# Kernel optimization log

Measured on AMD Instinct MI355X. Metric: run time of the kernel, lower is better.

The kernel has to match this reference:

```python
import jax, jax.numpy as jnp
import numpy as np

EMBED_DIM = 1024
NUM_HEADS = 16
HEAD_DIM = EMBED_DIM // NUM_HEADS
N, S = 4, 2048


def setup_inputs() -> dict:
    key = jax.random.key(0)
    ks = jax.random.split(key, 11)
    s = 1.0 / np.sqrt(EMBED_DIM)
    inp = {
        'query': jax.random.normal(ks[0], (N, S, EMBED_DIM), jnp.float32),
        'key': jax.random.normal(ks[1], (N, S, EMBED_DIM), jnp.float32),
        'value': jax.random.normal(ks[2], (N, S, EMBED_DIM), jnp.float32),
        'wq': jax.random.normal(ks[3], (EMBED_DIM, EMBED_DIM), jnp.float32) * s,
        'bq': jnp.zeros((EMBED_DIM,), jnp.float32),
        'wk': jax.random.normal(ks[4], (EMBED_DIM, EMBED_DIM), jnp.float32) * s,
        'bk': jnp.zeros((EMBED_DIM,), jnp.float32),
        'wv': jax.random.normal(ks[5], (EMBED_DIM, EMBED_DIM), jnp.float32) * s,
        'bv': jnp.zeros((EMBED_DIM,), jnp.float32),
        'wo': jax.random.normal(ks[6], (EMBED_DIM, EMBED_DIM), jnp.float32) * s,
        'bo': jnp.zeros((EMBED_DIM,), jnp.float32),
    }
    return inp


def reference(query, key, value, wq, bq, wk, bk, wv, bv, wo, bo):
    n = query.shape[0]
    # projections: y = x @ W^T + b (torch nn.Linear convention)
    Q = query @ wq.T + bq
    K = key @ wk.T + bk
    V = value @ wv.T + bv
    # [n, h, s, d]
    Q = Q.reshape(n, -1, NUM_HEADS, HEAD_DIM).transpose(0, 2, 1, 3)
    K = K.reshape(n, -1, NUM_HEADS, HEAD_DIM).transpose(0, 2, 1, 3)
    V = V.reshape(n, -1, NUM_HEADS, HEAD_DIM).transpose(0, 2, 1, 3)
    energy = jnp.einsum('nhqd,nhkd->nhqk', Q, K)
    attn = jax.nn.softmax(energy / jnp.sqrt(jnp.float32(HEAD_DIM)), axis=-1)
    out = jnp.einsum('nhqk,nhkd->nhqd', attn, V)
    out = out.transpose(0, 2, 1, 3).reshape(n, -1, NUM_HEADS * HEAD_DIM)
    return out @ wo.T + bo
```

## Files before the change

### kernel.cpp

```cpp
#include <hip/hip_runtime.h>
#include <hip/hip_bf16.h>

#define EMBED 1024
#define SEQ   2048
#define NB    4
#define NH    16
#define HD    64
#define MROWS (NB*SEQ)

typedef __attribute__((ext_vector_type(4))) float  f32x4;
typedef __attribute__((ext_vector_type(8))) short  s16x8;

#define MFMA16(a,b,c) __builtin_amdgcn_mfma_f32_16x16x32_bf16((a),(b),(c),0,0,0)

__device__ __forceinline__ unsigned short f2bf(float f) {
    union { float f; unsigned int u; } v; v.f = f;
    unsigned int r = v.u + 0x7fffu + ((v.u >> 16) & 1u);
    return (unsigned short)(r >> 16);
}
__device__ __forceinline__ unsigned int cvtpk(float a, float b) {
    unsigned int r;
    asm("v_cvt_pk_bf16_f32 %0, %1, %2" : "=v"(r) : "v"(a), "v"(b));
    return r;
}
__device__ __forceinline__ float exp2r(float x) {
    float r;
    asm("v_exp_f32 %0, %1" : "=v"(r) : "v"(x));
    return r;
}
__device__ __forceinline__ int swz(int row, int colb) {
    return row*128 + (colb ^ ((row & 7) << 4));
}

#define SC2 0.18033688f

template<int OMODE, int SCALEQ>
__global__ __launch_bounds__(256) void gemm_proj(
    const float* __restrict__ Af, const float* __restrict__ W,
    const float* __restrict__ bias, unsigned short* __restrict__ Yb)
{
    __shared__ unsigned short Ald[128*72];
    __shared__ unsigned short Bld[128*72];
    const int t   = threadIdx.x;
    const int bm  = blockIdx.x, bn = blockIdx.y;
    const int wid = t >> 6, lane = t & 63, l15 = lane & 15, blk = lane >> 4;
    const int wr  = wid >> 1, wc = wid & 1;

    f32x4 acc[4][4] = {};

    for (int kt = 0; kt < EMBED/64; ++kt) {
        #pragma unroll
        for (int i = 0; i < 8; ++i) {
            int f = t + 256*i, row = f >> 4, c4 = f & 15;
            float4 v = *(const float4*)(Af + (size_t)(bm*128+row)*EMBED + kt*64 + c4*4);
            *(uint2*)&Ald[row*72 + c4*4] = make_uint2(cvtpk(v.x,v.y), cvtpk(v.z,v.w));
        }
        #pragma unroll
        for (int i = 0; i < 8; ++i) {
            int f = t + 256*i, row = f >> 4, c4 = f & 15;
            float4 v = *(const float4*)(W + (size_t)(bn*128+row)*EMBED + kt*64 + c4*4);
            *(uint2*)&Bld[row*72 + c4*4] = make_uint2(cvtpk(v.x,v.y), cvtpk(v.z,v.w));
        }
        __syncthreads();
        #pragma unroll
        for (int ks = 0; ks < 2; ++ks) {
            s16x8 af[4], bf[4];
            #pragma unroll
            for (int mt = 0; mt < 4; ++mt)
                af[mt] = *(const s16x8*)&Ald[(wr*64 + mt*16 + l15)*72 + ks*32 + blk*8];
            #pragma unroll
            for (int nt = 0; nt < 4; ++nt)
                bf[nt] = *(const s16x8*)&Bld[(wc*64 + nt*16 + l15)*72 + ks*32 + blk*8];
            #pragma unroll
            for (int mt = 0; mt < 4; ++mt)
                #pragma unroll
                for (int nt = 0; nt < 4; ++nt)
                    acc[mt][nt] = MFMA16(af[mt], bf[nt], acc[mt][nt]);
        }
        __syncthreads();
    }

    float bv4[4];
    #pragma unroll
    for (int nt = 0; nt < 4; ++nt)
        bv4[nt] = bias[bn*128 + wc*64 + nt*16 + l15];

    #pragma unroll
    for (int mt = 0; mt < 4; ++mt) {
        #pragma unroll
        for (int nt = 0; nt < 4; ++nt) {
            const int m0 = bm*128 + wr*64 + mt*16 + blk*4;
            const int n  = bn*128 + wc*64 + nt*16 + l15;
            f32x4 a = acc[mt][nt];
            if (OMODE == 0) {
                #pragma unroll
                for (int r = 0; r < 4; ++r) {
                    float val = a[r] + bv4[nt];
                    if (SCALEQ) val *= SC2;
                    Yb[(size_t)(m0+r)*EMBED + n] = f2bf(val);
                }
            } else {
                const int b = m0 >> 11, s = m0 & (SEQ-1);
                const int h = n >> 6,  d = n & (HD-1);
                ushort4 pk;
                pk.x = f2bf(a[0] + bv4[nt]); pk.y = f2bf(a[1] + bv4[nt]);
                pk.z = f2bf(a[2] + bv4[nt]); pk.w = f2bf(a[3] + bv4[nt]);
                *(ushort4*)&Yb[(((size_t)b*NH + h)*HD + d)*SEQ + s] = pk;
            }
        }
    }
}

__global__ __launch_bounds__(256) void gemm_out(
    const unsigned short* __restrict__ Ab, const float* __restrict__ W,
    const float* __restrict__ bias, float* __restrict__ Yf)
{
    __shared__ unsigned short Ald[128*72];
    __shared__ unsigned short Bld[128*72];
    const int t   = threadIdx.x;
    const int bm  = blockIdx.x, bn = blockIdx.y;
    const int wid = t >> 6, lane = t & 63, l15 = lane & 15, blk = lane >> 4;
    const int wr  = wid >> 1, wc = wid & 1;

    f32x4 acc[4][4] = {};

    for (int kt = 0; kt < EMBED/64; ++kt) {
        #pragma unroll
        for (int i = 0; i < 4; ++i) {
            int f = t + 256*i, row = f >> 3, c8 = f & 7;
            *(s16x8*)&Ald[row*72 + c8*8] =
                *(const s16x8*)(Ab + (size_t)(bm*128+row)*EMBED + kt*64 + c8*8);
        }
        #pragma unroll
        for (int i = 0; i < 8; ++i) {
            int f = t + 256*i, row = f >> 4, c4 = f & 15;
            float4 v = *(const float4*)(W + (size_t)(bn*128+row)*EMBED + kt*64 + c4*4);
            *(uint2*)&Bld[row*72 + c4*4] = make_uint2(cvtpk(v.x,v.y), cvtpk(v.z,v.w));
        }
        __syncthreads();
        #pragma unroll
        for (int ks = 0; ks < 2; ++ks) {
            s16x8 af[4], bf[4];
            #pragma unroll
            for (int mt = 0; mt < 4; ++mt)
                af[mt] = *(const s16x8*)&Ald[(wr*64 + mt*16 + l15)*72 + ks*32 + blk*8];
            #pragma unroll
            for (int nt = 0; nt < 4; ++nt)
                bf[nt] = *(const s16x8*)&Bld[(wc*64 + nt*16 + l15)*72 + ks*32 + blk*8];
            #pragma unroll
            for (int mt = 0; mt < 4; ++mt)
                #pragma unroll
                for (int nt = 0; nt < 4; ++nt)
                    acc[mt][nt] = MFMA16(af[mt], bf[nt], acc[mt][nt]);
        }
        __syncthreads();
    }

    float bv4[4];
    #pragma unroll
    for (int nt = 0; nt < 4; ++nt)
        bv4[nt] = bias[bn*128 + wc*64 + nt*16 + l15];

    #pragma unroll
    for (int mt = 0; mt < 4; ++mt)
        #pragma unroll
        for (int nt = 0; nt < 4; ++nt) {
            const int m0 = bm*128 + wr*64 + mt*16 + blk*4;
            const int n  = bn*128 + wc*64 + nt*16 + l15;
            f32x4 a = acc[mt][nt];
            #pragma unroll
            for (int r = 0; r < 4; ++r)
                Yf[(size_t)(m0+r)*EMBED + n] = a[r] + bv4[nt];
        }
}

__global__ __launch_bounds__(256) void attn_fwd(
    const unsigned short* __restrict__ Qp,
    const unsigned short* __restrict__ Kp,
    const unsigned short* __restrict__ Vt,
    unsigned short* __restrict__ ctx)
{
    __shared__ unsigned short Kld[64*64];
    __shared__ unsigned short Vld[64*64];
    __shared__ unsigned short Pld[4][32*64];

    const int t = threadIdx.x, wid = t >> 6, lane = t & 63;
    const int l15 = lane & 15, blk = lane >> 4;
    const int bh = blockIdx.x, qb = blockIdx.y;
    const int b = bh >> 4, h = bh & (NH-1);
    const int q0 = qb*128 + wid*32;

    s16x8 qf[2][2];
    #pragma unroll
    for (int qs = 0; qs < 2; ++qs) {
        const unsigned short* qp = Qp + (size_t)(b*SEQ + q0 + qs*16 + l15)*EMBED + h*HD;
        qf[qs][0] = *(const s16x8*)(qp + blk*8);
        qf[qs][1] = *(const s16x8*)(qp + 32 + blk*8);
    }

    const unsigned short* kb = Kp + (size_t)b*SEQ*EMBED + h*HD;
    const unsigned short* vb = Vt + (size_t)bh*HD*SEQ;

    const int srow = t >> 3, scolb = (t & 7)*16;
    const unsigned short* kg0 = kb + (size_t)srow*EMBED + scolb/2;
    const unsigned short* kg1 = kb + (size_t)(srow+32)*EMBED + scolb/2;
    const unsigned short* vg0 = vb + (size_t)srow*SEQ + scolb/2;
    const unsigned short* vg1 = vb + (size_t)(srow+32)*SEQ + scolb/2;
    const int w0 = swz(srow, scolb), w1 = swz(srow+32, scolb);

    unsigned short* pl = &Pld[wid][0];
    const int rc0 = (blk*16) ^ ((l15 & 7) << 4);
    const int rc1 = rc0 ^ 64;

    s16x8 onesf;
    #pragma unroll
    for (int i = 0; i < 8; ++i) onesf[i] = (short)0x3F80;

    f32x4 o[2][4] = {};
    f32x4 sacc[2] = {};

    s16x8 kr0 = *(const s16x8*)kg0;
    s16x8 kr1 = *(const s16x8*)kg1;
    s16x8 vr0 = *(const s16x8*)vg0;
    s16x8 vr1 = *(const s16x8*)vg1;

    for (int tt = 0; tt < SEQ/64; ++tt) {
        __syncthreads();
        *(s16x8*)((char*)Kld + w0) = kr0;
        *(s16x8*)((char*)Kld + w1) = kr1;
        *(s16x8*)((char*)Vld + w0) = vr0;
        *(s16x8*)((char*)Vld + w1) = vr1;
        __syncthreads();
        if (tt + 1 < SEQ/64) {
            const size_t ko = (size_t)(tt+1)*64;
            kr0 = *(const s16x8*)(kg0 + ko*EMBED);
            kr1 = *(const s16x8*)(kg1 + ko*EMBED);
            vr0 = *(const s16x8*)(vg0 + ko);
            vr1 = *(const s16x8*)(vg1 + ko);
        }

        f32x4 sc[2][4];
        #pragma unroll
        for (int qs = 0; qs < 2; ++qs)
            #pragma unroll
            for (int kt = 0; kt < 4; ++kt)
                sc[qs][kt] = f32x4{0.f,0.f,0.f,0.f};
        __builtin_amdgcn_s_setprio(1);
        #pragma unroll
        for (int kt = 0; kt < 4; ++kt) {
            const char* krow = (const char*)Kld + (kt*16 + l15)*128;
            s16x8 ka0 = *(const s16x8*)(krow + rc0);
            s16x8 ka1 = *(const s16x8*)(krow + rc1);
            #pragma unroll
            for (int qs = 0; qs < 2; ++qs) {
                sc[qs][kt] = MFMA16(ka0, qf[qs][0], sc[qs][kt]);
                sc[qs][kt] = MFMA16(ka1, qf[qs][1], sc[qs][kt]);
            }
        }
        __builtin_amdgcn_s_setprio(0);

        #pragma unroll
        for (int qs = 0; qs < 2; ++qs) {
            #pragma unroll
            for (int kt = 0; kt < 4; ++kt) {
                const float e0 = exp2r(sc[qs][kt][0]);
                const float e1 = exp2r(sc[qs][kt][1]);
                const float e2 = exp2r(sc[qs][kt][2]);
                const float e3 = exp2r(sc[qs][kt][3]);
                const int off = (qs*16 + l15)*128 + ((kt*32 + blk*8) ^ ((l15 & 7) << 4));
                *(uint2*)((char*)pl + off) = make_uint2(cvtpk(e0,e1), cvtpk(e2,e3));
            }
        }

        s16x8 pa[2][2];
        #pragma unroll
        for (int qs = 0; qs < 2; ++qs) {
            const char* prow = (const char*)pl + (qs*16 + l15)*128;
            pa[qs][0] = *(const s16x8*)(prow + rc0);
            pa[qs][1] = *(const s16x8*)(prow + rc1);
        }
        __builtin_amdgcn_s_setprio(1);
        #pragma unroll
        for (int qs = 0; qs < 2; ++qs) {
            sacc[qs] = MFMA16(pa[qs][0], onesf, sacc[qs]);
            sacc[qs] = MFMA16(pa[qs][1], onesf, sacc[qs]);
        }
        #pragma unroll
        for (int dt = 0; dt < 4; ++dt) {
            const char* vrow = (const char*)Vld + (dt*16 + l15)*128;
            s16x8 vb0 = *(const s16x8*)(vrow + rc0);
            s16x8 vb1 = *(const s16x8*)(vrow + rc1);
            #pragma unroll
            for (int qs = 0; qs < 2; ++qs) {
                o[qs][dt] = MFMA16(pa[qs][0], vb0, o[qs][dt]);
                o[qs][dt] = MFMA16(pa[qs][1], vb1, o[qs][dt]);
            }
        }
        __builtin_amdgcn_s_setprio(0);
    }

    #pragma unroll
    for (int qs = 0; qs < 2; ++qs) {
        float li[4];
        #pragma unroll
        for (int r = 0; r < 4; ++r) li[r] = 1.f / sacc[qs][r];
        unsigned short* cp = ctx + (size_t)(b*SEQ + q0 + qs*16)*EMBED + h*HD;
        #pragma unroll
        for (int dt = 0; dt < 4; ++dt)
            #pragma unroll
            for (int r = 0; r < 4; ++r)
                cp[(size_t)(blk*4 + r)*EMBED + dt*16 + l15] = f2bf(o[qs][dt][r] * li[r]);
    }
}

extern "C" void kernel_launch(void* const* d_in, const int* in_sizes, int n_in,
                              void* d_out, int out_size, void* d_ws, size_t ws_size,
                              hipStream_t stream)
{
    const float* q  = (const float*)d_in[0];
    const float* k  = (const float*)d_in[1];
    const float* v  = (const float*)d_in[2];
    const float* wq = (const float*)d_in[3];
    const float* bq = (const float*)d_in[4];
    const float* wk = (const float*)d_in[5];
    const float* bk = (const float*)d_in[6];
    const float* wv = (const float*)d_in[7];
    const float* bv = (const float*)d_in[8];
    const float* wo = (const float*)d_in[9];
    const float* bo = (const float*)d_in[10];

    unsigned short* Qp  = (unsigned short*)d_out;
    unsigned short* Kp  = Qp + (size_t)MROWS*EMBED;
    unsigned short* Vt  = (unsigned short*)d_ws;
    unsigned short* ctx = Vt + (size_t)MROWS*EMBED;
    float* out = (float*)d_out;

    dim3 g(MROWS/128, EMBED/128), tpb(256);
    gemm_proj<0,1><<<g, tpb, 0, stream>>>(q, wq, bq, Qp);
    gemm_proj<0,0><<<g, tpb, 0, stream>>>(k, wk, bk, Kp);
    gemm_proj<1,0><<<g, tpb, 0, stream>>>(v, wv, bv, Vt);
    attn_fwd<<<dim3(NB*NH, SEQ/128), tpb, 0, stream>>>(Qp, Kp, Vt, ctx);
    gemm_out<<<dim3(MROWS/128, EMBED/128), tpb, 0, stream>>>(ctx, wo, bo, out);
}
```

Measured before the change: 224.7 us.

## Double-buffer K/V tiles with direct global-to-LDS loads in attention

Replaces the register-staged K/V tile loads in the attention kernel with global_load_lds (direct global-to-LDS) into two LDS buffers, prefetching the next tile while the current one is computed. The XOR swizzle moves from the LDS write address to the global source address, and the loop uses one barrier per iteration instead of two. This aims to cut register pressure and barrier overhead and to overlap memory with MFMA work, at the cost of doubling K/V LDS usage, which can reduce occupancy.

```diff
diff --git a/kernel.cpp b/kernel.cpp
--- a/kernel.cpp
+++ b/kernel.cpp
@@ -27,6 +27,11 @@
     float r;
     asm("v_exp_f32 %0, %1" : "=v"(r) : "v"(x));
     return r;
+}
+__device__ __forceinline__ void gload16(const void* g, void* l) {
+    __builtin_amdgcn_global_load_lds(
+        (const __attribute__((address_space(1))) void*)g,
+        (__attribute__((address_space(3))) void*)l, 16, 0, 0);
 }
 __device__ __forceinline__ int swz(int row, int colb) {
     return row*128 + (colb ^ ((row & 7) << 4));
@@ -180,8 +185,8 @@
     const unsigned short* __restrict__ Vt,
     unsigned short* __restrict__ ctx)
 {
-    __shared__ unsigned short Kld[64*64];
-    __shared__ unsigned short Vld[64*64];
+    __shared__ unsigned short Kld[2][64*64];
+    __shared__ unsigned short Vld[2][64*64];
     __shared__ unsigned short Pld[4][32*64];
 
     const int t = threadIdx.x, wid = t >> 6, lane = t & 63;
@@ -201,12 +206,15 @@
     const unsigned short* kb = Kp + (size_t)b*SEQ*EMBED + h*HD;
     const unsigned short* vb = Vt + (size_t)bh*HD*SEQ;
 
-    const int srow = t >> 3, scolb = (t & 7)*16;
-    const unsigned short* kg0 = kb + (size_t)srow*EMBED + scolb/2;
-    const unsigned short* kg1 = kb + (size_t)(srow+32)*EMBED + scolb/2;
-    const unsigned short* vg0 = vb + (size_t)srow*SEQ + scolb/2;
-    const unsigned short* vg1 = vb + (size_t)(srow+32)*SEQ + scolb/2;
-    const int w0 = swz(srow, scolb), w1 = swz(srow+32, scolb);
+    const int c0 = wid*2, c1 = wid*2 + 1;
+    const int u0 = c0*64 + lane,              u1 = c1*64 + lane;
+    const int r0 = u0 >> 3,                   r1 = u1 >> 3;
+    const int s0 = ((((u0&7)<<4) ^ ((r0&7)<<4)) >> 1);
+    const int s1 = ((((u1&7)<<4) ^ ((r1&7)<<4)) >> 1);
+    const unsigned short* kS0 = kb + (size_t)r0*EMBED + s0;
+    const unsigned short* kS1 = kb + (size_t)r1*EMBED + s1;
+    const unsigned short* vS0 = vb + (size_t)r0*SEQ  + s0;
+    const unsigned short* vS1 = vb + (size_t)r1*SEQ  + s1;
 
     unsigned short* pl = &Pld[wid][0];
     const int rc0 = (blk*16) ^ ((l15 & 7) << 4);
@@ -219,25 +227,27 @@
     f32x4 o[2][4] = {};
     f32x4 sacc[2] = {};
 
-    s16x8 kr0 = *(const s16x8*)kg0;
-    s16x8 kr1 = *(const s16x8*)kg1;
-    s16x8 vr0 = *(const s16x8*)vg0;
-    s16x8 vr1 = *(const s16x8*)vg1;
-
+    gload16(kS0, (char*)Kld[0] + c0*1024);
+    gload16(kS1, (char*)Kld[0] + c1*1024);
+    gload16(vS0, (char*)Vld[0] + c0*1024);
+    gload16(vS1, (char*)Vld[0] + c1*1024);
+    asm volatile("s_waitcnt vmcnt(0)" ::: "memory");
+    __syncthreads();
+
+    int cur = 0;
     for (int tt = 0; tt < SEQ/64; ++tt) {
-        __syncthreads();
-        *(s16x8*)((char*)Kld + w0) = kr0;
-        *(s16x8*)((char*)Kld + w1) = kr1;
-        *(s16x8*)((char*)Vld + w0) = vr0;
-        *(s16x8*)((char*)Vld + w1) = vr1;
-        __syncthreads();
         if (tt + 1 < SEQ/64) {
             const size_t ko = (size_t)(tt+1)*64;
-            kr0 = *(const s16x8*)(kg0 + ko*EMBED);
-            kr1 = *(const s16x8*)(kg1 + ko*EMBED);
-            vr0 = *(const s16x8*)(vg0 + ko);
-            vr1 = *(const s16x8*)(vg1 + ko);
-        }
+            char* kd = (char*)Kld[cur^1];
+            char* vd = (char*)Vld[cur^1];
+            gload16(kS0 + ko*EMBED, kd + c0*1024);
+            gload16(kS1 + ko*EMBED, kd + c1*1024);
+            gload16(vS0 + ko,       vd + c0*1024);
+            gload16(vS1 + ko,       vd + c1*1024);
+        }
+
+        const char* kbase = (const char*)Kld[cur];
+        const char* vbase = (const char*)Vld[cur];
 
         f32x4 sc[2][4];
         #pragma unroll
@@ -248,7 +258,7 @@
         __builtin_amdgcn_s_setprio(1);
         #pragma unroll
         for (int kt = 0; kt < 4; ++kt) {
-            const char* krow = (const char*)Kld + (kt*16 + l15)*128;
+            const char* krow = kbase + (kt*16 + l15)*128;
             s16x8 ka0 = *(const s16x8*)(krow + rc0);
             s16x8 ka1 = *(const s16x8*)(krow + rc1);
             #pragma unroll
@@ -287,7 +297,7 @@
         }
         #pragma unroll
         for (int dt = 0; dt < 4; ++dt) {
-            const char* vrow = (const char*)Vld + (dt*16 + l15)*128;
+            const char* vrow = vbase + (dt*16 + l15)*128;
             s16x8 vb0 = *(const s16x8*)(vrow + rc0);
             s16x8 vb1 = *(const s16x8*)(vrow + rc1);
             #pragma unroll
@@ -297,6 +307,10 @@
             }
         }
         __builtin_amdgcn_s_setprio(0);
+
+        asm volatile("s_waitcnt vmcnt(0)" ::: "memory");
+        __syncthreads();
+        cur ^= 1;
     }
 
     #pragma unroll
```

Result: no change. 220.7 us (-1.8%).
